# Performance work log

Hardware: AMD Instinct MI355X
Metric: run time of the kernel (lower is better)

Reference implementation:

```python
import jax, jax.numpy as jnp
import numpy as np

BETA = 0.95      # leak
THRESH = 1.0     # snntorch Leaky default threshold
ALPHA = 2.0      # ATan surrogate alpha (atan_with_alpha)
T = 100          # SPIKE_STEPS
D_IN = 65536     # input_dims
HID = 256        # fc1 hidden (hardcoded)
N_OUT = 20       # n_actions(2) * NUM_NEURONS_PER_ACTION(10)


def spike_fn(x):
    # forward of snntorch surrogate.ATan: Heaviside
    return (x > 0.0).astype(x.dtype)


def lif_step(mem, cur):
    # snntorch Leaky, reset_mechanism='subtract':
    # reset computed from previous membrane (detached), then decay+integrate, then fire
    reset = jax.lax.stop_gradient((mem > THRESH).astype(mem.dtype))
    mem_new = BETA * mem + cur - reset * THRESH
    spk = spike_fn(mem_new - THRESH)
    return spk, mem_new


def _run_net(x, W1, b1, W2, b2):
    # x: [T, D_IN]. Precompute all layer-1 currents as one big GEMM, then scan the recurrence.
    cur1_all = x @ W1.T + b1  # [T, HID]

    def step(carry, cur1):
        mem1, mem2 = carry
        spk1, mem1 = lif_step(mem1, cur1)
        cur2 = spk1 @ W2.T + b2  # [n_out]
        spk2, mem2 = lif_step(mem2, cur2)
        return (mem1, mem2), spk2

    init = (jnp.zeros((W1.shape[0],), x.dtype), jnp.zeros((W2.shape[0],), x.dtype))
    (_, mem2_final), spk2_hist = jax.lax.scan(step, init, cur1_all)
    return spk2_hist, mem2_final  # [T, n_out], [n_out]


def setup_inputs() -> dict:
    key = jax.random.key(0)
    ks = jax.random.split(key, 5)
    s = 0.01
    return {
        "poisson_spikes": jax.random.uniform(ks[0], (T, 1, D_IN), dtype=jnp.float32),
        "aW1": jax.random.normal(ks[1], (HID, D_IN), dtype=jnp.float32) * s,
        "ab1": jnp.zeros((HID,), jnp.float32),
        "aW2": jax.random.normal(ks[2], (N_OUT, HID), dtype=jnp.float32) * s,
        "ab2": jnp.zeros((N_OUT,), jnp.float32),
        "cW1": jax.random.normal(ks[3], (HID, D_IN), dtype=jnp.float32) * s,
        "cb1": jnp.zeros((HID,), jnp.float32),
        "cW2": jax.random.normal(ks[4], (1, HID), dtype=jnp.float32) * s,
        "cb2": jnp.zeros((1,), jnp.float32),
    }


def reference(poisson_spikes, aW1, ab1, aW2, ab2, cW1, cb1, cW2, cb2):
    x = poisson_spikes[:, 0, :]  # effective batch of 1 -> [T, D_IN]
    actor_spk_hist, _ = _run_net(x, aW1, ab1, aW2, ab2)        # [T, 20]
    _, critic_mem = _run_net(x, cW1, cb1, cW2, cb2)            # [1]
    spk_sum = actor_spk_hist.sum(axis=0)                       # [20] (sum over timesteps)
    action_vals = jnp.stack([spk_sum[:10].sum(), spk_sum[10:].sum()])
    policy = jax.nn.softmax(action_vals)                       # [2]
    return policy, critic_mem
```

## Files before the change

kernel.cpp:

```cpp
#include <hip/hip_runtime.h>
#include <hip/hip_bf16.h>

#define T_STEPS 100
#define D_IN    65536
#define HID     256
#define HTOT    512
#define BETA    0.95f
#define THRESH  1.0f

typedef __bf16 bf16x8 __attribute__((ext_vector_type(8)));
typedef float  f32x16 __attribute__((ext_vector_type(16)));

__device__ __forceinline__ void gload_lds16(const void* g, void* l) {
    __builtin_amdgcn_global_load_lds(
        (const __attribute__((address_space(1))) void*)g,
        (__attribute__((address_space(3))) void*)l, 16, 0, 0);
}

__global__ __launch_bounds__(512) void k_xpack(
    const float* __restrict__ x, __bf16* __restrict__ xp)
{
    const int idx  = blockIdx.x * 512 + threadIdx.x;
    const int slot = idx & 3;
    const int r    = (idx >> 2) & 127;
    const int gk   = idx >> 9;

    float f[8] = {0.f, 0.f, 0.f, 0.f, 0.f, 0.f, 0.f, 0.f};
    if (r < T_STEPS) {
        const float* src = x + (size_t)r * D_IN + gk * 32 + slot * 8;
        float4 v0 = *(const float4*)src;
        float4 v1 = *(const float4*)(src + 4);
        f[0] = v0.x; f[1] = v0.y; f[2] = v0.z; f[3] = v0.w;
        f[4] = v1.x; f[5] = v1.y; f[6] = v1.z; f[7] = v1.w;
    }
    bf16x8 hi, mi;
#pragma unroll
    for (int e = 0; e < 8; e++) {
        __bf16 h = (__bf16)f[e];
        hi[e] = h; mi[e] = (__bf16)(f[e] - (float)h);
    }
    const int G = r * 4 + (slot ^ ((r >> 1) & 3));
    __bf16* blob = xp + (size_t)gk * 8192;
    *(bf16x8*)(blob + G * 8)        = hi;
    *(bf16x8*)(blob + 4096 + G * 8) = mi;
}

__global__ __launch_bounds__(256, 2) void k_gemm1(
    const float* __restrict__ aW1,
    const float* __restrict__ cW1,
    const __bf16* __restrict__ xp,
    float* __restrict__ P,
    int nsteps)
{
    const int d    = blockIdx.x;
    const int xcd  = d & 7;
    const int sl   = d >> 3;
    const int s    = xcd * 16 + (sl & 15);
    const int ht   = sl >> 4;

    const int tid  = threadIdx.x;
    const int lane = tid & 63;
    const int l31  = lane & 31;
    const int h5   = lane >> 5;
    const int wv   = tid >> 6;
    const int wt   = (wv & 1) * 64;
    const int wh   = (wv >> 1) * 64;

    __shared__ __align__(16) char smem[2][32768];

    const float* Wbase = (ht < 2) ? (aW1 + (size_t)ht * 128 * D_IN)
                                  : (cW1 + (size_t)(ht - 2) * 128 * D_IN);

    const float* wsrc[4];
#pragma unroll
    for (int o = 0; o < 4; o++) {
        const int idx = o * 256 + tid;
        const int row = idx >> 3, wj = idx & 7;
        wsrc[o] = Wbase + (size_t)row * D_IN + (wj ^ (row & 7)) * 4;
    }
    const int gk0 = s * nsteps;

    f32x16 acc00, acc01, acc10, acc11;
#pragma unroll
    for (int i = 0; i < 16; i++) {
        acc00[i] = 0.f; acc01[i] = 0.f; acc10[i] = 0.f; acc11[i] = 0.f;
    }

#define STAGE(i) do {                                                         \
    char* b_ = smem[(i) & 1];                                                 \
    const __bf16* xb_ = xp + (size_t)(gk0 + (i)) * 8192;                      \
    const int kc_ = (gk0 + (i)) * 32;                                         \
    _Pragma("unroll")                                                         \
    for (int o = 0; o < 4; o++) {                                             \
        const int g_ = o * 256 + tid;                                         \
        gload_lds16(xb_ + g_ * 8, b_ + g_ * 16);                              \
    }                                                                         \
    _Pragma("unroll")                                                         \
    for (int o = 0; o < 4; o++) {                                             \
        const int g_ = o * 256 + tid;                                         \
        gload_lds16(wsrc[o] + kc_, b_ + 16384 + g_ * 16);                     \
    }                                                                         \
} while (0)

#define CVT8(dsth, dstm, va, vb) do {                                         \
    float f_[8] = {va.x, va.y, va.z, va.w, vb.x, vb.y, vb.z, vb.w};           \
    _Pragma("unroll")                                                         \
    for (int e = 0; e < 8; e++) {                                             \
        __bf16 h = (__bf16)f_[e];                                             \
        dsth[e] = h; dstm[e] = (__bf16)(f_[e] - (float)h);                    \
    }                                                                         \
} while (0)

#define COMPUTE(i) do {                                                       \
    const char* b_ = smem[(i) & 1];                                           \
    _Pragma("unroll")                                                         \
    for (int s16 = 0; s16 < 2; s16++) {                                       \
                                           \
        const int slot_ = s16 * 2 + h5;                                       \
        const int r0 = wt + l31, r1 = r0 + 32;                                \
        const int G0 = r0 * 4 + (slot_ ^ ((r0 >> 1) & 3));                    \
        const int G1 = r1 * 4 + (slot_ ^ ((r1 >> 1) & 3));                    \
        bf16x8 a0h = *(const bf16x8*)(b_ + G0 * 16);                          \
        bf16x8 a0m = *(const bf16x8*)(b_ + 8192 + G0 * 16);                   \
        bf16x8 a1h = *(const bf16x8*)(b_ + G1 * 16);                          \
        bf16x8 a1m = *(const bf16x8*)(b_ + 8192 + G1 * 16);                   \
                      \
        const int gb = s16 * 4 + h5 * 2;                                      \
        const int hrA = wh + l31, hrB = hrA + 32;                             \
        const char* wrA_ = b_ + 16384 + hrA * 128;                            \
        const char* wrB_ = b_ + 16384 + hrB * 128;                            \
        float4 waA = *(const float4*)(wrA_ + ((gb ^ (hrA & 7)) * 16));        \
        float4 wbA = *(const float4*)(wrA_ + (((gb + 1) ^ (hrA & 7)) * 16));  \
        float4 waB = *(const float4*)(wrB_ + ((gb ^ (hrB & 7)) * 16));        \
        float4 wbB = *(const float4*)(wrB_ + (((gb + 1) ^ (hrB & 7)) * 16));  \
        bf16x8 bhA, bmA, bhB, bmB;                                            \
        CVT8(bhA, bmA, waA, wbA);                                             \
        CVT8(bhB, bmB, waB, wbB);                                             \
        acc00 = __builtin_amdgcn_mfma_f32_32x32x16_bf16(a0m, bhA, acc00, 0,0,0); \
        acc00 = __builtin_amdgcn_mfma_f32_32x32x16_bf16(a0h, bmA, acc00, 0,0,0); \
        acc00 = __builtin_amdgcn_mfma_f32_32x32x16_bf16(a0h, bhA, acc00, 0,0,0); \
        acc01 = __builtin_amdgcn_mfma_f32_32x32x16_bf16(a0m, bhB, acc01, 0,0,0); \
        acc01 = __builtin_amdgcn_mfma_f32_32x32x16_bf16(a0h, bmB, acc01, 0,0,0); \
        acc01 = __builtin_amdgcn_mfma_f32_32x32x16_bf16(a0h, bhB, acc01, 0,0,0); \
        acc10 = __builtin_amdgcn_mfma_f32_32x32x16_bf16(a1m, bhA, acc10, 0,0,0); \
        acc10 = __builtin_amdgcn_mfma_f32_32x32x16_bf16(a1h, bmA, acc10, 0,0,0); \
        acc10 = __builtin_amdgcn_mfma_f32_32x32x16_bf16(a1h, bhA, acc10, 0,0,0); \
        acc11 = __builtin_amdgcn_mfma_f32_32x32x16_bf16(a1m, bhB, acc11, 0,0,0); \
        acc11 = __builtin_amdgcn_mfma_f32_32x32x16_bf16(a1h, bmB, acc11, 0,0,0); \
        acc11 = __builtin_amdgcn_mfma_f32_32x32x16_bf16(a1h, bhB, acc11, 0,0,0); \
    }                                                                         \
} while (0)

    STAGE(0);
    STAGE(1);
    for (int i = 0; i < nsteps; i++) {
        if (i + 1 < nsteps) asm volatile("s_waitcnt vmcnt(8)" ::: "memory");
        else                asm volatile("s_waitcnt vmcnt(0)" ::: "memory");
        __builtin_amdgcn_s_barrier();
        __builtin_amdgcn_sched_barrier(0);
        COMPUTE(i);
        __builtin_amdgcn_s_barrier();
        __builtin_amdgcn_sched_barrier(0);
        if (i + 2 < nsteps) STAGE(i + 2);
    }
#undef STAGE
#undef CVT8
#undef COMPUTE

    const int rbase = 4 * h5;
    float* Pb = P + (size_t)s * T_STEPS * HTOT;
    const int hA = ht * 128 + wh + l31;
    const int hB = hA + 32;
#pragma unroll
    for (int reg = 0; reg < 16; reg++) {
        const int row = (reg & 3) + rbase + 8 * (reg >> 2);
        const int t0  = wt + row;
        const int t1  = wt + 32 + row;
        if (t0 < T_STEPS) {
            Pb[(size_t)t0 * HTOT + hA] = acc00[reg];
            Pb[(size_t)t0 * HTOT + hB] = acc01[reg];
        }
        if (t1 < T_STEPS) {
            Pb[(size_t)t1 * HTOT + hA] = acc10[reg];
            Pb[(size_t)t1 * HTOT + hB] = acc11[reg];
        }
    }
}

__global__ __launch_bounds__(256) void k_reduce(
    const float* __restrict__ P,
    const float* __restrict__ ab1, const float* __restrict__ cb1,
    float* __restrict__ cur1, int NS)
{
    int g4 = blockIdx.x * 256 + threadIdx.x;
    int g  = g4 * 4;
    int h0 = g & (HTOT - 1);
    float4 sum;
    sum.x = (h0 + 0 < HID) ? ab1[h0 + 0] : cb1[h0 + 0 - HID];
    sum.y = (h0 + 1 < HID) ? ab1[h0 + 1] : cb1[h0 + 1 - HID];
    sum.z = (h0 + 2 < HID) ? ab1[h0 + 2] : cb1[h0 + 2 - HID];
    sum.w = (h0 + 3 < HID) ? ab1[h0 + 3] : cb1[h0 + 3 - HID];
    for (int ss = 0; ss < NS; ss++) {
        float4 v = *(const float4*)(P + (size_t)ss * T_STEPS * HTOT + g);
        sum.x += v.x; sum.y += v.y; sum.z += v.z; sum.w += v.w;
    }
    *(float4*)(cur1 + g) = sum;
}

__global__ __launch_bounds__(64) void k_lif1(
    const float* __restrict__ cur1,
    unsigned long long* __restrict__ bitsws,
    float* __restrict__ wsa)
{
    const int b    = blockIdx.x;
    const int lane = threadIdx.x;
    const int n    = b * 64 + lane;

    float mem = 0.f;
    for (int tb = 0; tb < T_STEPS; tb += 10) {
        float c[10];
#pragma unroll
        for (int i = 0; i < 10; i++) c[i] = cur1[(size_t)(tb + i) * HTOT + n];
#pragma unroll
        for (int i = 0; i < 10; i++) {
            float reset = (mem > THRESH) ? THRESH : 0.f;
            mem = BETA * mem + c[i] - reset;
            unsigned long long m = __ballot(mem > THRESH);
            if (lane == 0) bitsws[(size_t)(tb + i) * 8 + b] = m;
        }
    }
    if (b == 0 && lane == 0) { wsa[0] = 0.f; wsa[1] = 0.f; }
}

__global__ __launch_bounds__(128) void k_gemm2(
    const unsigned long long* __restrict__ bitsws,
    const float* __restrict__ aW2, const float* __restrict__ ab2,
    const float* __restrict__ cW2, const float* __restrict__ cb2,
    float* __restrict__ wsa, float* __restrict__ out)
{
    const int j   = blockIdx.x;
    const int tid = threadIdx.x;

    __shared__ float W[256];
    __shared__ float c2[T_STEPS];

    const float* Wsrc = (j < 20) ? (aW2 + j * 256) : cW2;
    for (int i = tid; i < 256; i += 128) W[i] = Wsrc[i];
    const float bias  = (j < 20) ? ab2[j] : cb2[0];
    const int   wbase = (j < 20) ? 0 : 4;
    __syncthreads();

    const int t = tid;
    if (t < T_STEPS) {
        unsigned long long m0 = bitsws[(size_t)t * 8 + wbase + 0];
        unsigned long long m1 = bitsws[(size_t)t * 8 + wbase + 1];
        unsigned long long m2 = bitsws[(size_t)t * 8 + wbase + 2];
        unsigned long long m3 = bitsws[(size_t)t * 8 + wbase + 3];
        float acc = bias;
#pragma unroll
        for (int bitp = 0; bitp < 64; bitp++) {
            acc += ((m0 >> bitp) & 1ULL) ? W[bitp]       : 0.f;
            acc += ((m1 >> bitp) & 1ULL) ? W[64 + bitp]  : 0.f;
            acc += ((m2 >> bitp) & 1ULL) ? W[128 + bitp] : 0.f;
            acc += ((m3 >> bitp) & 1ULL) ? W[192 + bitp] : 0.f;
        }
        c2[t] = acc;
    }
    __syncthreads();

    if (tid == 0) {
        float mem = 0.f, spk = 0.f;
        for (int tt = 0; tt < T_STEPS; tt++) {
            float reset = (mem > THRESH) ? THRESH : 0.f;
            mem = BETA * mem + c2[tt] - reset;
            spk += (mem > THRESH) ? 1.f : 0.f;
        }
        if (j < 10)       atomicAdd(&wsa[0], spk);
        else if (j < 20)  atomicAdd(&wsa[1], spk);
        else              out[2] = mem;
    }
}

__global__ __launch_bounds__(64) void k_final(
    const float* __restrict__ wsa, float* __restrict__ out)
{
    if (threadIdx.x == 0) {
        float a0 = wsa[0], a1 = wsa[1];
        float mx = fmaxf(a0, a1);
        float e0 = expf(a0 - mx), e1 = expf(a1 - mx);
        float inv = 1.f / (e0 + e1);
        out[0] = e0 * inv;
        out[1] = e1 * inv;
    }
}

extern "C" void kernel_launch(void* const* d_in, const int* in_sizes, int n_in,
                              void* d_out, int out_size, void* d_ws, size_t ws_size,
                              hipStream_t stream) {
    const float* x   = (const float*)d_in[0];
    const float* aW1 = (const float*)d_in[1];
    const float* ab1 = (const float*)d_in[2];
    const float* aW2 = (const float*)d_in[3];
    const float* ab2 = (const float*)d_in[4];
    const float* cW1 = (const float*)d_in[5];
    const float* cb1 = (const float*)d_in[6];
    const float* cW2 = (const float*)d_in[7];
    const float* cb2 = (const float*)d_in[8];
    float* out = (float*)d_out;

    const size_t xpack_bytes = 2048ull * 16384;
    const int NS = 128;
    const int nsteps = (D_IN / NS) / 32;

    __bf16* xpack = (__bf16*)d_ws;
    float*  P     = (float*)((char*)d_ws + xpack_bytes);
    float*  cur1  = P + (size_t)NS * T_STEPS * HTOT;
    unsigned long long* bitsws =
        (unsigned long long*)(cur1 + T_STEPS * HTOT);
    float* wsa = (float*)(bitsws + T_STEPS * 8);

    k_xpack <<<2048, 512, 0, stream>>>(x, xpack);
    k_gemm1 <<<512, 256, 0, stream>>>(aW1, cW1, xpack, P, nsteps);
    k_reduce<<<(T_STEPS * HTOT / 4) / 256, 256, 0, stream>>>(P, ab1, cb1, cur1, NS);
    k_lif1  <<<8, 64, 0, stream>>>(cur1, bitsws, wsa);
    k_gemm2 <<<21, 128, 0, stream>>>(bitsws, aW2, ab2, cW2, cb2, wsa, out);
    k_final <<<1, 64, 0, stream>>>(wsa, out);
}
```

Measured before the change: 97.47 us.

## Fuse x bf16 split packing into GEMM1 by loading fp32 x directly

Removes the separate k_xpack kernel that wrote the hi/lo bf16 split of x to workspace, and instead has k_gemm1 load fp32 x rows straight into LDS with the same XOR swizzle as W, converting to hi/mid bf16 in registers before the MFMAs. This drops one launch and the 32MB packed-x round trip through memory. In exchange, every GEMM block re-converts x (each x tile is read by the four h-tile blocks), which adds conversion ALU work and raises x global reads from bf16 pack size to fp32, with padded rows clamped to row 99.

```diff
diff --git a/kernel.cpp b/kernel.cpp
--- a/kernel.cpp
+++ b/kernel.cpp
@@ -17,38 +17,10 @@
         (__attribute__((address_space(3))) void*)l, 16, 0, 0);
 }
 
-__global__ __launch_bounds__(512) void k_xpack(
-    const float* __restrict__ x, __bf16* __restrict__ xp)
-{
-    const int idx  = blockIdx.x * 512 + threadIdx.x;
-    const int slot = idx & 3;
-    const int r    = (idx >> 2) & 127;
-    const int gk   = idx >> 9;
-
-    float f[8] = {0.f, 0.f, 0.f, 0.f, 0.f, 0.f, 0.f, 0.f};
-    if (r < T_STEPS) {
-        const float* src = x + (size_t)r * D_IN + gk * 32 + slot * 8;
-        float4 v0 = *(const float4*)src;
-        float4 v1 = *(const float4*)(src + 4);
-        f[0] = v0.x; f[1] = v0.y; f[2] = v0.z; f[3] = v0.w;
-        f[4] = v1.x; f[5] = v1.y; f[6] = v1.z; f[7] = v1.w;
-    }
-    bf16x8 hi, mi;
-#pragma unroll
-    for (int e = 0; e < 8; e++) {
-        __bf16 h = (__bf16)f[e];
-        hi[e] = h; mi[e] = (__bf16)(f[e] - (float)h);
-    }
-    const int G = r * 4 + (slot ^ ((r >> 1) & 3));
-    __bf16* blob = xp + (size_t)gk * 8192;
-    *(bf16x8*)(blob + G * 8)        = hi;
-    *(bf16x8*)(blob + 4096 + G * 8) = mi;
-}
-
 __global__ __launch_bounds__(256, 2) void k_gemm1(
     const float* __restrict__ aW1,
     const float* __restrict__ cW1,
-    const __bf16* __restrict__ xp,
+    const float* __restrict__ x,
     float* __restrict__ P,
     int nsteps)
 {
@@ -71,12 +43,15 @@
     const float* Wbase = (ht < 2) ? (aW1 + (size_t)ht * 128 * D_IN)
                                   : (cW1 + (size_t)(ht - 2) * 128 * D_IN);
 
+    const float* xsrc[4];
     const float* wsrc[4];
 #pragma unroll
     for (int o = 0; o < 4; o++) {
         const int idx = o * 256 + tid;
-        const int row = idx >> 3, wj = idx & 7;
-        wsrc[o] = Wbase + (size_t)row * D_IN + (wj ^ (row & 7)) * 4;
+        const int row = idx >> 3, g = idx & 7;
+        const int xrow = (row < T_STEPS) ? row : (T_STEPS - 1);
+        xsrc[o] = x     + (size_t)xrow * D_IN + (g ^ (row & 7)) * 4;
+        wsrc[o] = Wbase + (size_t)row  * D_IN + (g ^ (row & 7)) * 4;
     }
     const int gk0 = s * nsteps;
 
@@ -88,12 +63,11 @@
 
 #define STAGE(i) do {                                                         \
     char* b_ = smem[(i) & 1];                                                 \
-    const __bf16* xb_ = xp + (size_t)(gk0 + (i)) * 8192;                      \
     const int kc_ = (gk0 + (i)) * 32;                                         \
     _Pragma("unroll")                                                         \
     for (int o = 0; o < 4; o++) {                                             \
         const int g_ = o * 256 + tid;                                         \
-        gload_lds16(xb_ + g_ * 8, b_ + g_ * 16);                              \
+        gload_lds16(xsrc[o] + kc_, b_ + g_ * 16);                             \
     }                                                                         \
     _Pragma("unroll")                                                         \
     for (int o = 0; o < 4; o++) {                                             \
@@ -115,17 +89,20 @@
     const char* b_ = smem[(i) & 1];                                           \
     _Pragma("unroll")                                                         \
     for (int s16 = 0; s16 < 2; s16++) {                                       \
-                                           \
         const int slot_ = s16 * 2 + h5;                                       \
+        const int gb    = slot_ * 2;                                          \
+            \
         const int r0 = wt + l31, r1 = r0 + 32;                                \
-        const int G0 = r0 * 4 + (slot_ ^ ((r0 >> 1) & 3));                    \
-        const int G1 = r1 * 4 + (slot_ ^ ((r1 >> 1) & 3));                    \
-        bf16x8 a0h = *(const bf16x8*)(b_ + G0 * 16);                          \
-        bf16x8 a0m = *(const bf16x8*)(b_ + 8192 + G0 * 16);                   \
-        bf16x8 a1h = *(const bf16x8*)(b_ + G1 * 16);                          \
-        bf16x8 a1m = *(const bf16x8*)(b_ + 8192 + G1 * 16);                   \
+        const char* xr0_ = b_ + r0 * 128;                                     \
+        const char* xr1_ = b_ + r1 * 128;                                     \
+        float4 xa0 = *(const float4*)(xr0_ + ((gb ^ (r0 & 7)) * 16));         \
+        float4 xb0 = *(const float4*)(xr0_ + (((gb + 1) ^ (r0 & 7)) * 16));   \
+        float4 xa1 = *(const float4*)(xr1_ + ((gb ^ (r1 & 7)) * 16));         \
+        float4 xb1 = *(const float4*)(xr1_ + (((gb + 1) ^ (r1 & 7)) * 16));   \
+        bf16x8 a0h, a0m, a1h, a1m;                                            \
+        CVT8(a0h, a0m, xa0, xb0);                                             \
+        CVT8(a1h, a1m, xa1, xb1);                                             \
                       \
-        const int gb = s16 * 4 + h5 * 2;                                      \
         const int hrA = wh + l31, hrB = hrA + 32;                             \
         const char* wrA_ = b_ + 16384 + hrA * 128;                            \
         const char* wrB_ = b_ + 16384 + hrB * 128;                            \
@@ -308,19 +285,16 @@
     const float* cb2 = (const float*)d_in[8];
     float* out = (float*)d_out;
 
-    const size_t xpack_bytes = 2048ull * 16384;
     const int NS = 128;
     const int nsteps = (D_IN / NS) / 32;
 
-    __bf16* xpack = (__bf16*)d_ws;
-    float*  P     = (float*)((char*)d_ws + xpack_bytes);
-    float*  cur1  = P + (size_t)NS * T_STEPS * HTOT;
+    float* P    = (float*)d_ws;
+    float* cur1 = P + (size_t)NS * T_STEPS * HTOT;
     unsigned long long* bitsws =
         (unsigned long long*)(cur1 + T_STEPS * HTOT);
     float* wsa = (float*)(bitsws + T_STEPS * 8);
 
-    k_xpack <<<2048, 512, 0, stream>>>(x, xpack);
-    k_gemm1 <<<512, 256, 0, stream>>>(aW1, cW1, xpack, P, nsteps);
+    k_gemm1 <<<512, 256, 0, stream>>>(aW1, cW1, x, P, nsteps);
     k_reduce<<<(T_STEPS * HTOT / 4) / 256, 256, 0, stream>>>(P, ab1, cb1, cur1, NS);
     k_lif1  <<<8, 64, 0, stream>>>(cur1, bitsws, wsa);
     k_gemm2 <<<21, 128, 0, stream>>>(bitsws, aW2, ab2, cW2, cb2, wsa, out);
```

Result: faster. 92.77 us (-4.8%).
